# Performance work log

Measured on AMD Instinct MI355X. Metric: run time of the kernel, lower is better.

The kernel has to match this reference:

```python
import jax, jax.numpy as jnp
import numpy as np

NUM_USER = 50000
NUM_ITEM = 30000
N_NODES = NUM_USER + NUM_ITEM
N_EDGES = 1_000_000
FEAT_DIM = 768
DIM_LATENT = 128
DIM_ID = 64
NEG_SLOPE = 0.01  # F.leaky_relu default


def leaky_relu(x):
    return jnp.where(x >= 0, x, NEG_SLOPE * x)


def l2_normalize(x, eps=1e-12):
    # F.normalize(dim=-1): divide by clamped L2 norm
    n = jnp.sqrt(jnp.sum(x * x, axis=-1, keepdims=True))
    return x / jnp.maximum(n, eps)


def graph_gat(x, W, edge_index, num_nodes):
    """MGAT GraphGAT: x -> x@W, gated inner-product attention, softmax over
    incoming edges per destination node, scatter-add, L2 normalize."""
    x = x @ W                                    # [N, D]
    src = edge_index[0]                          # j (source)
    dst = edge_index[1]                          # i (target)
    x_j = x[src]                                 # [E, D]
    x_i = x[dst]                                 # [E, D]
    inner = jnp.sum(x_i * x_j, axis=-1)          # [E]
    # gate: sigmoid(deg(src)^-0.5 * inner)
    deg = jax.ops.segment_sum(jnp.ones_like(inner), src, num_segments=num_nodes)
    gate = jax.nn.sigmoid(deg[src] ** -0.5 * inner)
    score = inner * gate                         # [E]
    # segment softmax over destination nodes
    smax = jax.ops.segment_max(score, dst, num_segments=num_nodes)
    e = jnp.exp(score - smax[dst])
    denom = jax.ops.segment_sum(e, dst, num_segments=num_nodes)
    alpha = e / (denom[dst] + 1e-16)             # [E]
    out = jax.ops.segment_sum(x_j * alpha[:, None], dst, num_segments=num_nodes)
    return l2_normalize(out)


def setup_inputs() -> dict:
    key = jax.random.key(0)
    ks = jax.random.split(key, 16)

    def xavier(k, shape):
        fan_in, fan_out = shape[0], shape[1]
        std = float(np.sqrt(2.0 / (fan_in + fan_out)))
        return jax.random.normal(k, shape, dtype=jnp.float32) * std

    features = jax.random.normal(ks[0], (NUM_ITEM, FEAT_DIM), dtype=jnp.float32)
    id_embedding = jax.random.normal(ks[1], (N_NODES, DIM_ID), dtype=jnp.float32)
    # edge_index [2, E] with no self-loops (remove_self_loops is then identity)
    src = jax.random.randint(ks[2], (N_EDGES,), 0, N_NODES)
    off = jax.random.randint(ks[3], (N_EDGES,), 1, N_NODES)
    dst = (src + off) % N_NODES
    edge_index = jnp.stack([src, dst]).astype(jnp.int64)

    return {
        "features": features,
        "id_embedding": id_embedding,
        "edge_index": edge_index,
        "preference": xavier(ks[4], (NUM_USER, DIM_LATENT)),
        "mlp_w": xavier(ks[5], (FEAT_DIM, DIM_LATENT)),
        "mlp_b": jnp.zeros((DIM_LATENT,), dtype=jnp.float32),
        "conv1_w": xavier(ks[6], (DIM_LATENT, DIM_LATENT)),
        "lin1_w": xavier(ks[7], (DIM_LATENT, DIM_ID)),
        "lin1_b": jnp.zeros((DIM_ID,), dtype=jnp.float32),
        "g1_w": xavier(ks[8], (DIM_LATENT, DIM_ID)),
        "g1_b": jnp.zeros((DIM_ID,), dtype=jnp.float32),
        "conv2_w": xavier(ks[9], (DIM_ID, DIM_ID)),
        "lin2_w": xavier(ks[10], (DIM_ID, DIM_ID)),
        "lin2_b": jnp.zeros((DIM_ID,), dtype=jnp.float32),
        "g2_w": xavier(ks[11], (DIM_ID, DIM_ID)),
        "g2_b": jnp.zeros((DIM_ID,), dtype=jnp.float32),
    }


def reference(features, id_embedding, edge_index, preference, mlp_w, mlp_b,
              conv1_w, lin1_w, lin1_b, g1_w, g1_b,
              conv2_w, lin2_w, lin2_b, g2_w, g2_b):
    temp_features = jnp.tanh(features @ mlp_w + mlp_b)        # [num_item, dim_latent]
    x = jnp.concatenate([preference, temp_features], axis=0)  # [N, dim_latent]
    x = l2_normalize(x)

    h = leaky_relu(graph_gat(x, conv1_w, edge_index, N_NODES))
    x_hat = leaky_relu(x @ lin1_w + lin1_b) + id_embedding
    x1 = leaky_relu(h @ g1_w + g1_b + x_hat)                  # [N, dim_id]

    h = leaky_relu(graph_gat(x1, conv2_w, edge_index, N_NODES))
    x_hat = leaky_relu(x1 @ lin2_w + lin2_b) + id_embedding
    x2 = leaky_relu(h @ g2_w + g2_b + x_hat)                  # [N, dim_id]

    return jnp.concatenate([x1, x2], axis=1)                  # [N, 2*dim_id]
```

## Files before the change

### kernel.cpp

```cpp
#include <hip/hip_runtime.h>
#include <hip/hip_bf16.h>
#include <math.h>

#define NUM_USER 50000
#define NUM_ITEM 30000
#define N_NODES  80000
#define N_EDGES  1000000
#define FEAT_DIM 768
#define DLAT 128
#define DID  64
#define NEG_SLOPE 0.01f

#define SCAN_NB ((N_NODES + 255) / 256)

__device__ __forceinline__ float leaky(float v) { return v >= 0.f ? v : NEG_SLOPE * v; }

__device__ __forceinline__ float wave_reduce_sum(float v) {
#pragma unroll
    for (int off = 32; off > 0; off >>= 1) v += __shfl_xor(v, off, 64);
    return v;
}

__device__ __forceinline__ unsigned short f2bf(float f) {
    unsigned int u = __float_as_uint(f);
    unsigned int r = u + 0x7fffu + ((u >> 16) & 1u);
    return (unsigned short)(r >> 16);
}
__device__ __forceinline__ float bf2f(unsigned short h) {
    return __uint_as_float(((unsigned int)h) << 16);
}

template<int K_TOTAL, int N_COLS, int ACT, bool HAS_BIAS>
__global__ __launch_bounds__(256) void gemm_kernel(
    const float* __restrict__ A, int lda,
    const float* __restrict__ W, const float* __restrict__ bias,
    float* __restrict__ O, int ldo, int rows)
{
    constexpr int KC = 64;
    constexpr int CT = N_COLS / 16;
    __shared__ float sW[KC * N_COLS];
    __shared__ float sX[64][KC + 4];

    const int tid = threadIdx.x;
    const int ty = tid >> 4;
    const int tx = tid & 15;
    const int r0 = blockIdx.x * 64;

    float acc[4][CT];
#pragma unroll
    for (int i = 0; i < 4; i++)
#pragma unroll
        for (int c = 0; c < CT; c++) acc[i][c] = 0.f;

    for (int kc = 0; kc < K_TOTAL; kc += KC) {
        const float4* Wc = (const float4*)(W + (size_t)kc * N_COLS);
        for (int i = tid; i < KC * N_COLS / 4; i += 256)
            ((float4*)sW)[i] = Wc[i];
        {
            int row = tid >> 2, q = tid & 3;
            int gr = r0 + row;
            float4 v[4];
            if (gr < rows) {
                const float4* Ar = (const float4*)(A + (size_t)gr * lda + kc);
#pragma unroll
                for (int i = 0; i < 4; i++) v[i] = Ar[q * 4 + i];
            } else {
#pragma unroll
                for (int i = 0; i < 4; i++) v[i] = make_float4(0.f, 0.f, 0.f, 0.f);
            }
#pragma unroll
            for (int i = 0; i < 4; i++)
                *(float4*)&sX[row][q * 16 + i * 4] = v[i];
        }
        __syncthreads();

        for (int k = 0; k < KC; k++) {
            float xv[4];
#pragma unroll
            for (int i = 0; i < 4; i++) xv[i] = sX[ty * 4 + i][k];
            float4 w0 = *(const float4*)&sW[k * N_COLS + tx * CT];
            if (CT == 8) {
                float4 w1 = *(const float4*)&sW[k * N_COLS + tx * CT + 4];
#pragma unroll
                for (int i = 0; i < 4; i++) {
                    acc[i][0] += xv[i] * w0.x; acc[i][1] += xv[i] * w0.y;
                    acc[i][2] += xv[i] * w0.z; acc[i][3] += xv[i] * w0.w;
                    acc[i][4] += xv[i] * w1.x; acc[i][5] += xv[i] * w1.y;
                    acc[i][6] += xv[i] * w1.z; acc[i][7] += xv[i] * w1.w;
                }
            } else {
#pragma unroll
                for (int i = 0; i < 4; i++) {
                    acc[i][0] += xv[i] * w0.x; acc[i][1] += xv[i] * w0.y;
                    acc[i][2] += xv[i] * w0.z; acc[i][3] += xv[i] * w0.w;
                }
            }
        }
        __syncthreads();
    }

#pragma unroll
    for (int i = 0; i < 4; i++) {
        int gr = r0 + ty * 4 + i;
        if (gr >= rows) continue;
#pragma unroll
        for (int c = 0; c < CT; c++) {
            int col = tx * CT + c;
            float v = acc[i][c];
            if (HAS_BIAS) v += bias[col];
            if (ACT == 1) v = tanhf(v);
            O[(size_t)gr * ldo + col] = v;
        }
    }
}

typedef __attribute__((ext_vector_type(8))) short short8v;
typedef __attribute__((ext_vector_type(4))) float f32x4;

__global__ __launch_bounds__(256) void wt_prep_kernel(
    const float* __restrict__ W, unsigned short* __restrict__ Wh,
    unsigned short* __restrict__ Wl)
{
    int id = blockIdx.x * 256 + threadIdx.x;
    if (id < FEAT_DIM * DLAT) {
        int n = id / FEAT_DIM, k = id % FEAT_DIM;
        float v = W[(size_t)k * DLAT + n];
        unsigned short h = f2bf(v);
        Wh[id] = h;
        Wl[id] = f2bf(v - bf2f(h));
    }
}

__global__ __launch_bounds__(256) void mlp_mfma_kernel(
    const float* __restrict__ F,
    const unsigned short* __restrict__ Wh, const unsigned short* __restrict__ Wl,
    const float* __restrict__ bias, float* __restrict__ xout)
{
    __shared__ unsigned short sAh[64][72];
    __shared__ unsigned short sAl[64][72];
    __shared__ unsigned short sWh[128][72];
    __shared__ unsigned short sWlo[128][72];

    const int tid = threadIdx.x;
    const int lane = tid & 63;
    const int w = tid >> 6;
    const int wr = w >> 1, wc = w & 1;
    const int r0 = blockIdx.x * 64;

    f32x4 acc[2][4];
#pragma unroll
    for (int m = 0; m < 2; m++)
#pragma unroll
        for (int n = 0; n < 4; n++) acc[m][n] = (f32x4){0.f, 0.f, 0.f, 0.f};

    for (int kc = 0; kc < FEAT_DIM; kc += 64) {
#pragma unroll
        for (int it = 0; it < 2; it++) {
            int slot = tid + it * 256;
            int row = slot >> 3;
            int k8 = (slot & 7) * 8;
            int gr = r0 + row;
            float v[8];
#pragma unroll
            for (int i = 0; i < 8; i++) v[i] = 0.f;
            if (gr < NUM_ITEM) {
                const float4* p = (const float4*)(F + (size_t)gr * FEAT_DIM + kc + k8);
                float4 a = p[0], b = p[1];
                v[0]=a.x; v[1]=a.y; v[2]=a.z; v[3]=a.w;
                v[4]=b.x; v[5]=b.y; v[6]=b.z; v[7]=b.w;
            }
            unsigned int ph[4], pl[4];
#pragma unroll
            for (int i = 0; i < 4; i++) {
                unsigned short h0 = f2bf(v[2*i]),   l0 = f2bf(v[2*i]   - bf2f(h0));
                unsigned short h1 = f2bf(v[2*i+1]), l1 = f2bf(v[2*i+1] - bf2f(h1));
                ph[i] = (unsigned int)h0 | ((unsigned int)h1 << 16);
                pl[i] = (unsigned int)l0 | ((unsigned int)l1 << 16);
            }
            *(int4*)&sAh[row][k8] = make_int4((int)ph[0], (int)ph[1], (int)ph[2], (int)ph[3]);
            *(int4*)&sAl[row][k8] = make_int4((int)pl[0], (int)pl[1], (int)pl[2], (int)pl[3]);
        }
#pragma unroll
        for (int it = 0; it < 4; it++) {
            int slot = tid + it * 256;
            int n = slot >> 3;
            int k8 = (slot & 7) * 8;
            *(int4*)&sWh[n][k8]  = *(const int4*)(Wh + (size_t)n * FEAT_DIM + kc + k8);
            *(int4*)&sWlo[n][k8] = *(const int4*)(Wl + (size_t)n * FEAT_DIM + kc + k8);
        }
        __syncthreads();

#pragma unroll
        for (int k0 = 0; k0 < 64; k0 += 32) {
            int klane = k0 + (lane >> 4) * 8;
            short8v ah[2], al[2], bh[4], bl[4];
#pragma unroll
            for (int m = 0; m < 2; m++) {
                int row = wr * 32 + m * 16 + (lane & 15);
                ah[m] = *(const short8v*)&sAh[row][klane];
                al[m] = *(const short8v*)&sAl[row][klane];
            }
#pragma unroll
            for (int n = 0; n < 4; n++) {
                int col = wc * 64 + n * 16 + (lane & 15);
                bh[n] = *(const short8v*)&sWh[col][klane];
                bl[n] = *(const short8v*)&sWlo[col][klane];
            }
#pragma unroll
            for (int m = 0; m < 2; m++)
#pragma unroll
                for (int n = 0; n < 4; n++) {
                    acc[m][n] = __builtin_amdgcn_mfma_f32_16x16x32_bf16(ah[m], bh[n], acc[m][n], 0, 0, 0);
                    acc[m][n] = __builtin_amdgcn_mfma_f32_16x16x32_bf16(ah[m], bl[n], acc[m][n], 0, 0, 0);
                    acc[m][n] = __builtin_amdgcn_mfma_f32_16x16x32_bf16(al[m], bh[n], acc[m][n], 0, 0, 0);
                }
        }
        __syncthreads();
    }

#pragma unroll
    for (int m = 0; m < 2; m++) {
        int rbase = r0 + wr * 32 + m * 16 + (lane >> 4) * 4;
#pragma unroll
        for (int n = 0; n < 4; n++) {
            int col = wc * 64 + n * 16 + (lane & 15);
            float bv = bias[col];
#pragma unroll
            for (int q = 0; q < 4; q++) {
                int gr = rbase + q;
                if (gr < NUM_ITEM)
                    xout[(size_t)gr * DLAT + col] = tanhf(acc[m][n][q] + bv);
            }
        }
    }
}

template<int K>
__global__ __launch_bounds__(256) void combine_gemm_kernel(
    const float* __restrict__ H,
    const float* __restrict__ X, int ldx,
    const float* __restrict__ g_w, const float* __restrict__ g_b,
    const float* __restrict__ lin_w, const float* __restrict__ lin_b,
    const float* __restrict__ id_emb,
    float* __restrict__ out, int out_off)
{
    constexpr int KC = 64;
    __shared__ float sWg[KC * DID];
    __shared__ float sWl[KC * DID];
    __shared__ float sH[64][KC + 4];
    __shared__ float sX[64][KC + 4];

    const int tid = threadIdx.x;
    const int ty = tid >> 4;
    const int tx = tid & 15;
    const int r0 = blockIdx.x * 64;

    float accG[4][4], accL[4][4];
#pragma unroll
    for (int i = 0; i < 4; i++)
#pragma unroll
        for (int c = 0; c < 4; c++) { accG[i][c] = 0.f; accL[i][c] = 0.f; }

    for (int kc = 0; kc < K; kc += KC) {
        const float4* Wg = (const float4*)(g_w + (size_t)kc * DID);
        const float4* Wl = (const float4*)(lin_w + (size_t)kc * DID);
        for (int i = tid; i < KC * DID / 4; i += 256) {
            ((float4*)sWg)[i] = Wg[i];
            ((float4*)sWl)[i] = Wl[i];
        }
        {
            int row = tid >> 2, q = tid & 3;
            int gr = r0 + row;
            const float4* Hr = (const float4*)(H + (size_t)gr * K + kc);
            const float4* Xr = (const float4*)(X + (size_t)gr * ldx + kc);
#pragma unroll
            for (int i = 0; i < 4; i++) {
                *(float4*)&sH[row][q * 16 + i * 4] = Hr[q * 4 + i];
                *(float4*)&sX[row][q * 16 + i * 4] = Xr[q * 4 + i];
            }
        }
        __syncthreads();

        for (int k = 0; k < KC; k++) {
            float hv[4], xv[4];
#pragma unroll
            for (int i = 0; i < 4; i++) { hv[i] = sH[ty * 4 + i][k]; xv[i] = sX[ty * 4 + i][k]; }
            float4 wg = *(const float4*)&sWg[k * DID + tx * 4];
            float4 wl = *(const float4*)&sWl[k * DID + tx * 4];
#pragma unroll
            for (int i = 0; i < 4; i++) {
                accG[i][0] += hv[i] * wg.x; accG[i][1] += hv[i] * wg.y;
                accG[i][2] += hv[i] * wg.z; accG[i][3] += hv[i] * wg.w;
                accL[i][0] += xv[i] * wl.x; accL[i][1] += xv[i] * wl.y;
                accL[i][2] += xv[i] * wl.z; accL[i][3] += xv[i] * wl.w;
            }
        }
        __syncthreads();
    }

#pragma unroll
    for (int i = 0; i < 4; i++) {
        int gr = r0 + ty * 4 + i;
#pragma unroll
        for (int c = 0; c < 4; c++) {
            int col = tx * 4 + c;
            float xh = leaky(accL[i][c] + lin_b[col]) + id_emb[(size_t)gr * DID + col];
            float v = leaky(accG[i][c] + g_b[col] + xh);
            out[(size_t)gr * (2 * DID) + out_off + col] = v;
        }
    }
}

__global__ __launch_bounds__(256) void l2norm_rows_kernel(float* __restrict__ x)
{
    int wid = blockIdx.x * 4 + (threadIdx.x >> 6);
    if (wid >= N_NODES) return;
    int lane = threadIdx.x & 63;
    float* row = x + (size_t)wid * DLAT;
    float v0 = row[lane], v1 = row[lane + 64];
    float s = wave_reduce_sum(v0 * v0 + v1 * v1);
    float inv = 1.0f / fmaxf(sqrtf(s), 1e-12f);
    row[lane] = v0 * inv;
    row[lane + 64] = v1 * inv;
}

__global__ __launch_bounds__(256) void count_kernel(
    const int* __restrict__ src, const int* __restrict__ dst,
    int* __restrict__ deg_out, int* __restrict__ cnt_in)
{
    int e = blockIdx.x * 256 + threadIdx.x;
    if (e < N_EDGES) {
        atomicAdd(&deg_out[src[e]], 1);
        atomicAdd(&cnt_in[dst[e]], 1);
    }
}

__global__ __launch_bounds__(256) void scan_local_kernel(
    const int* __restrict__ cnt, int* __restrict__ rowptr, int* __restrict__ blocksum)
{
    __shared__ int wsum[4];
    int gid = blockIdx.x * 256 + threadIdx.x;
    int lane = threadIdx.x & 63, w = threadIdx.x >> 6;
    int orig = (gid < N_NODES) ? cnt[gid] : 0;
    int v = orig;
#pragma unroll
    for (int off = 1; off < 64; off <<= 1) {
        int u = __shfl_up(v, off, 64);
        if (lane >= off) v += u;
    }
    if (lane == 63) wsum[w] = v;
    __syncthreads();
    int woff = 0;
#pragma unroll
    for (int i = 0; i < 4; i++) woff += (i < w) ? wsum[i] : 0;
    if (gid < N_NODES) rowptr[gid] = v - orig + woff;
    if (threadIdx.x == 255) blocksum[blockIdx.x] = woff + v;
}

__global__ __launch_bounds__(512) void scan_blocksums_kernel(int* __restrict__ blocksum)
{
    __shared__ int s[512];
    int t = threadIdx.x;
    int orig = (t < SCAN_NB) ? blocksum[t] : 0;
    s[t] = orig;
    __syncthreads();
    for (int off = 1; off < 512; off <<= 1) {
        int u = (t >= off) ? s[t - off] : 0;
        __syncthreads();
        s[t] += u;
        __syncthreads();
    }
    if (t < SCAN_NB) blocksum[t] = s[t] - orig;
}

__global__ __launch_bounds__(256) void scan_add_kernel(
    int* __restrict__ rowptr, const int* __restrict__ blocksum)
{
    int gid = blockIdx.x * 256 + threadIdx.x;
    if (gid < N_NODES) rowptr[gid] += blocksum[blockIdx.x];
    if (gid == 0) rowptr[N_NODES] = N_EDGES;
}

__global__ __launch_bounds__(256) void csr_fill_kernel(
    const int* __restrict__ src, const int* __restrict__ dst,
    const int* __restrict__ rowptr, int* __restrict__ cursor, int* __restrict__ csr_src)
{
    int e = blockIdx.x * 256 + threadIdx.x;
    if (e < N_EDGES) {
        int d = dst[e];
        int slot = rowptr[d] + atomicAdd(&cursor[d], 1);
        csr_src[slot] = src[e];
    }
}

__global__ __launch_bounds__(256) void deg_rsqrt_kernel(
    const int* __restrict__ deg_out, float* __restrict__ rsq)
{
    int n = blockIdx.x * 256 + threadIdx.x;
    if (n < N_NODES) rsq[n] = rsqrtf((float)deg_out[n]);
}

template<int D>
__global__ __launch_bounds__(256) void gat_layer_kernel(
    const float* __restrict__ xw, const int* __restrict__ rowptr,
    const int* __restrict__ csr_src, const float* __restrict__ rsq_deg,
    float* __restrict__ h)
{
    constexpr int SG  = D / 8;
    constexpr int EPC = 64 / SG;
    int wid = blockIdx.x * 4 + (threadIdx.x >> 6);
    if (wid >= N_NODES) return;
    const int lane = threadIdx.x & 63;
    const int g = lane / SG;
    const int t = lane % SG;
    const int start = rowptr[wid], end = rowptr[wid + 1];

    const float* xdp = xw + (size_t)wid * D + 8 * t;
    float4 xd0 = *(const float4*)(xdp);
    float4 xd1 = *(const float4*)(xdp + 4);

    float m = -1e30f, l = 0.f;
    float acc[8];
#pragma unroll
    for (int c = 0; c < 8; c++) acc[c] = 0.f;

    for (int base = start; base < end; base += EPC) {
        int i = base + g;
        bool valid = (i < end);
        int s = valid ? csr_src[i] : 0;
        const float* row = xw + (size_t)s * D + 8 * t;
        float4 a0 = *(const float4*)(row);
        float4 a1 = *(const float4*)(row + 4);
        float p = a0.x * xd0.x + a0.y * xd0.y + a0.z * xd0.z + a0.w * xd0.w
                + a1.x * xd1.x + a1.y * xd1.y + a1.z * xd1.z + a1.w * xd1.w;
#pragma unroll
        for (int off = SG / 2; off > 0; off >>= 1) p += __shfl_xor(p, off, 64);
        float rsd = valid ? rsq_deg[s] : 1.f;
        float gate = 1.0f / (1.0f + __expf(-(p * rsd)));
        float sc = valid ? p * gate : -1e30f;
        float mnew = fmaxf(m, sc);
        float scale = __expf(m - mnew);
        float w = valid ? __expf(sc - mnew) : 0.f;
        l = l * scale + w;
        acc[0] = acc[0] * scale + w * a0.x;
        acc[1] = acc[1] * scale + w * a0.y;
        acc[2] = acc[2] * scale + w * a0.z;
        acc[3] = acc[3] * scale + w * a0.w;
        acc[4] = acc[4] * scale + w * a1.x;
        acc[5] = acc[5] * scale + w * a1.y;
        acc[6] = acc[6] * scale + w * a1.z;
        acc[7] = acc[7] * scale + w * a1.w;
        m = mnew;
    }

#pragma unroll
    for (int off = SG; off < 64; off <<= 1) {
        float mo = __shfl_xor(m, off, 64);
        float lo = __shfl_xor(l, off, 64);
        float mnew = fmaxf(m, mo);
        float s1 = __expf(m - mnew), s2 = __expf(mo - mnew);
        l = l * s1 + lo * s2;
#pragma unroll
        for (int c = 0; c < 8; c++) {
            float ao = __shfl_xor(acc[c], off, 64);
            acc[c] = acc[c] * s1 + ao * s2;
        }
        m = mnew;
    }

    float invl = 1.0f / (l + 1e-16f);
    float ss = 0.f;
#pragma unroll
    for (int c = 0; c < 8; c++) { acc[c] *= invl; ss += acc[c] * acc[c]; }
#pragma unroll
    for (int off = SG / 2; off > 0; off >>= 1) ss += __shfl_xor(ss, off, 64);
    float inv = 1.0f / fmaxf(sqrtf(ss), 1e-12f);

    if (g == 0) {
        float4 o0, o1;
        o0.x = leaky(acc[0] * inv); o0.y = leaky(acc[1] * inv);
        o0.z = leaky(acc[2] * inv); o0.w = leaky(acc[3] * inv);
        o1.x = leaky(acc[4] * inv); o1.y = leaky(acc[5] * inv);
        o1.z = leaky(acc[6] * inv); o1.w = leaky(acc[7] * inv);
        float* op = h + (size_t)wid * D + 8 * t;
        *(float4*)(op) = o0;
        *(float4*)(op + 4) = o1;
    }
}

extern "C" void kernel_launch(void* const* d_in, const int* in_sizes, int n_in,
                              void* d_out, int out_size, void* d_ws, size_t ws_size,
                              hipStream_t stream)
{
    const float* features = (const float*)d_in[0];
    const float* id_emb   = (const float*)d_in[1];
    const int*   ei       = (const int*)d_in[2];
    const float* pref     = (const float*)d_in[3];
    const float* mlp_w    = (const float*)d_in[4];
    const float* mlp_b    = (const float*)d_in[5];
    const float* conv1_w  = (const float*)d_in[6];
    const float* lin1_w   = (const float*)d_in[7];
    const float* lin1_b   = (const float*)d_in[8];
    const float* g1_w     = (const float*)d_in[9];
    const float* g1_b     = (const float*)d_in[10];
    const float* conv2_w  = (const float*)d_in[11];
    const float* lin2_w   = (const float*)d_in[12];
    const float* lin2_b   = (const float*)d_in[13];
    const float* g2_w     = (const float*)d_in[14];
    const float* g2_b     = (const float*)d_in[15];
    const int* src = ei;
    const int* dst = ei + N_EDGES;
    float* out = (float*)d_out;

    float* x       = (float*)d_ws;
    float* xw      = x   + (size_t)N_NODES * DLAT;
    float* gat     = xw  + (size_t)N_NODES * DLAT;
    int*   deg_out = (int*)(gat + (size_t)N_NODES * DLAT);
    int*   cnt     = deg_out + N_NODES;
    int*   rowptr  = cnt + N_NODES;
    int*   csr_src = rowptr + N_NODES + 1;
    int*   blocksum = csr_src + N_EDGES;
    float* rsq_deg = (float*)cnt;
    unsigned short* Wh = (unsigned short*)gat;
    unsigned short* Wl = Wh + (size_t)FEAT_DIM * DLAT;

    hipMemsetAsync(deg_out, 0, N_NODES * sizeof(int), stream);
    hipMemsetAsync(cnt, 0, N_NODES * sizeof(int), stream);
    count_kernel<<<(N_EDGES + 255) / 256, 256, 0, stream>>>(src, dst, deg_out, cnt);
    scan_local_kernel<<<SCAN_NB, 256, 0, stream>>>(cnt, rowptr, blocksum);
    scan_blocksums_kernel<<<1, 512, 0, stream>>>(blocksum);
    scan_add_kernel<<<SCAN_NB, 256, 0, stream>>>(rowptr, blocksum);
    hipMemsetAsync(cnt, 0, N_NODES * sizeof(int), stream);
    csr_fill_kernel<<<(N_EDGES + 255) / 256, 256, 0, stream>>>(src, dst, rowptr, cnt, csr_src);
    deg_rsqrt_kernel<<<(N_NODES + 255) / 256, 256, 0, stream>>>(deg_out, rsq_deg);

    hipMemcpyAsync(x, pref, (size_t)NUM_USER * DLAT * sizeof(float),
                   hipMemcpyDeviceToDevice, stream);
    wt_prep_kernel<<<(FEAT_DIM * DLAT + 255) / 256, 256, 0, stream>>>(mlp_w, Wh, Wl);
    mlp_mfma_kernel<<<(NUM_ITEM + 63) / 64, 256, 0, stream>>>(
        features, Wh, Wl, mlp_b, x + (size_t)NUM_USER * DLAT);
    l2norm_rows_kernel<<<(N_NODES + 3) / 4, 256, 0, stream>>>(x);

    gemm_kernel<DLAT, DLAT, 0, false><<<N_NODES / 64, 256, 0, stream>>>(
        x, DLAT, conv1_w, nullptr, xw, DLAT, N_NODES);
    gat_layer_kernel<DLAT><<<(N_NODES + 3) / 4, 256, 0, stream>>>(
        xw, rowptr, csr_src, rsq_deg, gat);
    combine_gemm_kernel<DLAT><<<N_NODES / 64, 256, 0, stream>>>(
        gat, x, DLAT, g1_w, g1_b, lin1_w, lin1_b, id_emb, out, 0);

    gemm_kernel<DID, DID, 0, false><<<N_NODES / 64, 256, 0, stream>>>(
        out, 2 * DID, conv2_w, nullptr, xw, DID, N_NODES);
    gat_layer_kernel<DID><<<(N_NODES + 3) / 4, 256, 0, stream>>>(
        xw, rowptr, csr_src, rsq_deg, gat);
    combine_gemm_kernel<DID><<<N_NODES / 64, 256, 0, stream>>>(
        gat, out, 2 * DID, g2_w, g2_b, lin2_w, lin2_b, id_emb, out, DID);
}
```

Before: 515.1 us.

## Move conv and combine GEMMs to split-bf16 MFMA kernels

Replaces the scalar FP32 shared-memory GEMMs for the conv1/conv2 projections and the fused lin/gate combine step with MFMA kernels. These use a three-term hi/lo bf16 split to keep near-FP32 accuracy. All small weight matrices are pre-transposed and split into bf16 hi/lo buffers placed in extra workspace after the CSR arrays. B fragments are read straight from global memory rather than staged in LDS. The aim is to cut FP32 FMA cost, at the price of three times the MFMA work plus extra prep launches.

Measured after the change: 517.8 us. No clear change (+0.5%).

```diff
diff --git a/kernel.cpp b/kernel.cpp
--- a/kernel.cpp
+++ b/kernel.cpp
@@ -30,104 +30,192 @@
     return __uint_as_float(((unsigned int)h) << 16);
 }
 
-template<int K_TOTAL, int N_COLS, int ACT, bool HAS_BIAS>
-__global__ __launch_bounds__(256) void gemm_kernel(
-    const float* __restrict__ A, int lda,
-    const float* __restrict__ W, const float* __restrict__ bias,
-    float* __restrict__ O, int ldo, int rows)
-{
-    constexpr int KC = 64;
-    constexpr int CT = N_COLS / 16;
-    __shared__ float sW[KC * N_COLS];
-    __shared__ float sX[64][KC + 4];
-
-    const int tid = threadIdx.x;
-    const int ty = tid >> 4;
-    const int tx = tid & 15;
-    const int r0 = blockIdx.x * 64;
-
-    float acc[4][CT];
-#pragma unroll
-    for (int i = 0; i < 4; i++)
-#pragma unroll
-        for (int c = 0; c < CT; c++) acc[i][c] = 0.f;
-
-    for (int kc = 0; kc < K_TOTAL; kc += KC) {
-        const float4* Wc = (const float4*)(W + (size_t)kc * N_COLS);
-        for (int i = tid; i < KC * N_COLS / 4; i += 256)
-            ((float4*)sW)[i] = Wc[i];
-        {
-            int row = tid >> 2, q = tid & 3;
-            int gr = r0 + row;
-            float4 v[4];
-            if (gr < rows) {
-                const float4* Ar = (const float4*)(A + (size_t)gr * lda + kc);
-#pragma unroll
-                for (int i = 0; i < 4; i++) v[i] = Ar[q * 4 + i];
-            } else {
-#pragma unroll
-                for (int i = 0; i < 4; i++) v[i] = make_float4(0.f, 0.f, 0.f, 0.f);
-            }
-#pragma unroll
-            for (int i = 0; i < 4; i++)
-                *(float4*)&sX[row][q * 16 + i * 4] = v[i];
-        }
-        __syncthreads();
-
-        for (int k = 0; k < KC; k++) {
-            float xv[4];
-#pragma unroll
-            for (int i = 0; i < 4; i++) xv[i] = sX[ty * 4 + i][k];
-            float4 w0 = *(const float4*)&sW[k * N_COLS + tx * CT];
-            if (CT == 8) {
-                float4 w1 = *(const float4*)&sW[k * N_COLS + tx * CT + 4];
-#pragma unroll
-                for (int i = 0; i < 4; i++) {
-                    acc[i][0] += xv[i] * w0.x; acc[i][1] += xv[i] * w0.y;
-                    acc[i][2] += xv[i] * w0.z; acc[i][3] += xv[i] * w0.w;
-                    acc[i][4] += xv[i] * w1.x; acc[i][5] += xv[i] * w1.y;
-                    acc[i][6] += xv[i] * w1.z; acc[i][7] += xv[i] * w1.w;
-                }
-            } else {
-#pragma unroll
-                for (int i = 0; i < 4; i++) {
-                    acc[i][0] += xv[i] * w0.x; acc[i][1] += xv[i] * w0.y;
-                    acc[i][2] += xv[i] * w0.z; acc[i][3] += xv[i] * w0.w;
-                }
-            }
-        }
-        __syncthreads();
-    }
-
-#pragma unroll
-    for (int i = 0; i < 4; i++) {
-        int gr = r0 + ty * 4 + i;
-        if (gr >= rows) continue;
-#pragma unroll
-        for (int c = 0; c < CT; c++) {
-            int col = tx * CT + c;
-            float v = acc[i][c];
-            if (HAS_BIAS) v += bias[col];
-            if (ACT == 1) v = tanhf(v);
-            O[(size_t)gr * ldo + col] = v;
-        }
-    }
-}
-
 typedef __attribute__((ext_vector_type(8))) short short8v;
 typedef __attribute__((ext_vector_type(4))) float f32x4;
 
-__global__ __launch_bounds__(256) void wt_prep_kernel(
+__device__ __forceinline__ void split_store8(
+    float4 a, float4 b, unsigned short* dh, unsigned short* dl)
+{
+    float v[8] = {a.x, a.y, a.z, a.w, b.x, b.y, b.z, b.w};
+    unsigned int ph[4], pl[4];
+#pragma unroll
+    for (int i = 0; i < 4; i++) {
+        unsigned short h0 = f2bf(v[2*i]),   l0 = f2bf(v[2*i]   - bf2f(h0));
+        unsigned short h1 = f2bf(v[2*i+1]), l1 = f2bf(v[2*i+1] - bf2f(h1));
+        ph[i] = (unsigned int)h0 | ((unsigned int)h1 << 16);
+        pl[i] = (unsigned int)l0 | ((unsigned int)l1 << 16);
+    }
+    *(int4*)dh = make_int4((int)ph[0], (int)ph[1], (int)ph[2], (int)ph[3]);
+    *(int4*)dl = make_int4((int)pl[0], (int)pl[1], (int)pl[2], (int)pl[3]);
+}
+
+template<int KK, int NN>
+__global__ __launch_bounds__(256) void wt_prep_g_kernel(
     const float* __restrict__ W, unsigned short* __restrict__ Wh,
     unsigned short* __restrict__ Wl)
 {
     int id = blockIdx.x * 256 + threadIdx.x;
-    if (id < FEAT_DIM * DLAT) {
-        int n = id / FEAT_DIM, k = id % FEAT_DIM;
-        float v = W[(size_t)k * DLAT + n];
+    if (id < KK * NN) {
+        int n = id / KK, k = id % KK;
+        float v = W[(size_t)k * NN + n];
         unsigned short h = f2bf(v);
         Wh[id] = h;
         Wl[id] = f2bf(v - bf2f(h));
+    }
+}
+
+template<int K, int NC>
+__global__ __launch_bounds__(256) void conv_mfma_kernel(
+    const float* __restrict__ X, int ldx,
+    const unsigned short* __restrict__ Wth, const unsigned short* __restrict__ Wtl,
+    float* __restrict__ O, int ldo)
+{
+    constexpr int NW = NC / 64;
+    constexpr int MW = 4 / NW;
+    constexpr int WROWS = 64 / MW;
+    constexpr int MF = WROWS / 16;
+    constexpr int KSTEPS = K / 32;
+    constexpr int KP = K + 8;
+
+    __shared__ unsigned short sAh[64][KP];
+    __shared__ unsigned short sAl[64][KP];
+
+    const int tid = threadIdx.x;
+    const int lane = tid & 63;
+    const int w = tid >> 6;
+    const int wr = w / NW, wc = w % NW;
+    const int r0 = blockIdx.x * 64;
+
+#pragma unroll
+    for (int it = 0; it < K / 32; it++) {
+        int slot = tid + it * 256;
+        int row = slot / (K / 8);
+        int k8 = (slot % (K / 8)) * 8;
+        const float4* p = (const float4*)(X + (size_t)(r0 + row) * ldx + k8);
+        split_store8(p[0], p[1], &sAh[row][k8], &sAl[row][k8]);
+    }
+    __syncthreads();
+
+    f32x4 acc[MF][4];
+#pragma unroll
+    for (int m = 0; m < MF; m++)
+#pragma unroll
+        for (int n = 0; n < 4; n++) acc[m][n] = (f32x4){0.f, 0.f, 0.f, 0.f};
+
+#pragma unroll
+    for (int ks = 0; ks < KSTEPS; ks++) {
+        int klane = ks * 32 + (lane >> 4) * 8;
+        short8v ah[MF], al[MF];
+#pragma unroll
+        for (int m = 0; m < MF; m++) {
+            int row = wr * WROWS + m * 16 + (lane & 15);
+            ah[m] = *(const short8v*)&sAh[row][klane];
+            al[m] = *(const short8v*)&sAl[row][klane];
+        }
+#pragma unroll
+        for (int n = 0; n < 4; n++) {
+            int col = wc * 64 + n * 16 + (lane & 15);
+            short8v bh = *(const short8v*)(Wth + (size_t)col * K + klane);
+            short8v bl = *(const short8v*)(Wtl + (size_t)col * K + klane);
+#pragma unroll
+            for (int m = 0; m < MF; m++) {
+                acc[m][n] = __builtin_amdgcn_mfma_f32_16x16x32_bf16(ah[m], bh, acc[m][n], 0, 0, 0);
+                acc[m][n] = __builtin_amdgcn_mfma_f32_16x16x32_bf16(ah[m], bl, acc[m][n], 0, 0, 0);
+                acc[m][n] = __builtin_amdgcn_mfma_f32_16x16x32_bf16(al[m], bh, acc[m][n], 0, 0, 0);
+            }
+        }
+    }
+
+#pragma unroll
+    for (int m = 0; m < MF; m++) {
+        int rbase = r0 + wr * WROWS + m * 16 + (lane >> 4) * 4;
+#pragma unroll
+        for (int n = 0; n < 4; n++) {
+            int col = wc * 64 + n * 16 + (lane & 15);
+#pragma unroll
+            for (int q = 0; q < 4; q++)
+                O[(size_t)(rbase + q) * ldo + col] = acc[m][n][q];
+        }
+    }
+}
+
+template<int K>
+__global__ __launch_bounds__(256) void combine_mfma_kernel(
+    const float* __restrict__ H, int ldh,
+    const float* __restrict__ X, int ldx,
+    const unsigned short* __restrict__ Gth, const unsigned short* __restrict__ Gtl,
+    const unsigned short* __restrict__ Lth, const unsigned short* __restrict__ Ltl,
+    const float* __restrict__ g_b, const float* __restrict__ lin_b,
+    const float* __restrict__ id_emb, float* __restrict__ out, int out_off)
+{
+    constexpr int KSTEPS = K / 32;
+    constexpr int KP = K + 8;
+
+    __shared__ unsigned short sHh[64][KP];
+    __shared__ unsigned short sHl[64][KP];
+    __shared__ unsigned short sXh[64][KP];
+    __shared__ unsigned short sXl[64][KP];
+
+    const int tid = threadIdx.x;
+    const int lane = tid & 63;
+    const int wr = tid >> 6;
+    const int r0 = blockIdx.x * 64;
+
+#pragma unroll
+    for (int it = 0; it < K / 32; it++) {
+        int slot = tid + it * 256;
+        int row = slot / (K / 8);
+        int k8 = (slot % (K / 8)) * 8;
+        const float4* ph = (const float4*)(H + (size_t)(r0 + row) * ldh + k8);
+        split_store8(ph[0], ph[1], &sHh[row][k8], &sHl[row][k8]);
+        const float4* px = (const float4*)(X + (size_t)(r0 + row) * ldx + k8);
+        split_store8(px[0], px[1], &sXh[row][k8], &sXl[row][k8]);
+    }
+    __syncthreads();
+
+    f32x4 accG[4], accL[4];
+#pragma unroll
+    for (int n = 0; n < 4; n++) {
+        accG[n] = (f32x4){0.f, 0.f, 0.f, 0.f};
+        accL[n] = (f32x4){0.f, 0.f, 0.f, 0.f};
+    }
+
+#pragma unroll
+    for (int ks = 0; ks < KSTEPS; ks++) {
+        int klane = ks * 32 + (lane >> 4) * 8;
+        int row = wr * 16 + (lane & 15);
+        short8v hh = *(const short8v*)&sHh[row][klane];
+        short8v hl = *(const short8v*)&sHl[row][klane];
+        short8v xh = *(const short8v*)&sXh[row][klane];
+        short8v xl = *(const short8v*)&sXl[row][klane];
+#pragma unroll
+        for (int n = 0; n < 4; n++) {
+            int col = n * 16 + (lane & 15);
+            short8v gh = *(const short8v*)(Gth + (size_t)col * K + klane);
+            short8v gl = *(const short8v*)(Gtl + (size_t)col * K + klane);
+            short8v lh = *(const short8v*)(Lth + (size_t)col * K + klane);
+            short8v ll = *(const short8v*)(Ltl + (size_t)col * K + klane);
+            accG[n] = __builtin_amdgcn_mfma_f32_16x16x32_bf16(hh, gh, accG[n], 0, 0, 0);
+            accG[n] = __builtin_amdgcn_mfma_f32_16x16x32_bf16(hh, gl, accG[n], 0, 0, 0);
+            accG[n] = __builtin_amdgcn_mfma_f32_16x16x32_bf16(hl, gh, accG[n], 0, 0, 0);
+            accL[n] = __builtin_amdgcn_mfma_f32_16x16x32_bf16(xh, lh, accL[n], 0, 0, 0);
+            accL[n] = __builtin_amdgcn_mfma_f32_16x16x32_bf16(xh, ll, accL[n], 0, 0, 0);
+            accL[n] = __builtin_amdgcn_mfma_f32_16x16x32_bf16(xl, lh, accL[n], 0, 0, 0);
+        }
+    }
+
+    int rbase = r0 + wr * 16 + (lane >> 4) * 4;
+#pragma unroll
+    for (int n = 0; n < 4; n++) {
+        int col = n * 16 + (lane & 15);
+        float gb = g_b[col], lb = lin_b[col];
+#pragma unroll
+        for (int q = 0; q < 4; q++) {
+            int gr = rbase + q;
+            float xhv = leaky(accL[n][q] + lb) + id_emb[(size_t)gr * DID + col];
+            float v = leaky(accG[n][q] + gb + xhv);
+            out[(size_t)gr * (2 * DID) + out_off + col] = v;
+        }
     }
 }
 
@@ -160,25 +248,12 @@
             int row = slot >> 3;
             int k8 = (slot & 7) * 8;
             int gr = r0 + row;
-            float v[8];
-#pragma unroll
-            for (int i = 0; i < 8; i++) v[i] = 0.f;
+            float4 a = make_float4(0.f, 0.f, 0.f, 0.f), b = a;
             if (gr < NUM_ITEM) {
                 const float4* p = (const float4*)(F + (size_t)gr * FEAT_DIM + kc + k8);
-                float4 a = p[0], b = p[1];
-                v[0]=a.x; v[1]=a.y; v[2]=a.z; v[3]=a.w;
-                v[4]=b.x; v[5]=b.y; v[6]=b.z; v[7]=b.w;
+                a = p[0]; b = p[1];
             }
-            unsigned int ph[4], pl[4];
-#pragma unroll
-            for (int i = 0; i < 4; i++) {
-                unsigned short h0 = f2bf(v[2*i]),   l0 = f2bf(v[2*i]   - bf2f(h0));
-                unsigned short h1 = f2bf(v[2*i+1]), l1 = f2bf(v[2*i+1] - bf2f(h1));
-                ph[i] = (unsigned int)h0 | ((unsigned int)h1 << 16);
-                pl[i] = (unsigned int)l0 | ((unsigned int)l1 << 16);
-            }
-            *(int4*)&sAh[row][k8] = make_int4((int)ph[0], (int)ph[1], (int)ph[2], (int)ph[3]);
-            *(int4*)&sAl[row][k8] = make_int4((int)pl[0], (int)pl[1], (int)pl[2], (int)pl[3]);
+            split_store8(a, b, &sAh[row][k8], &sAl[row][k8]);
         }
 #pragma unroll
         for (int it = 0; it < 4; it++) {
@@ -231,82 +306,6 @@
                 if (gr < NUM_ITEM)
                     xout[(size_t)gr * DLAT + col] = tanhf(acc[m][n][q] + bv);
             }
-        }
-    }
-}
-
-template<int K>
-__global__ __launch_bounds__(256) void combine_gemm_kernel(
-    const float* __restrict__ H,
-    const float* __restrict__ X, int ldx,
-    const float* __restrict__ g_w, const float* __restrict__ g_b,
-    const float* __restrict__ lin_w, const float* __restrict__ lin_b,
-    const float* __restrict__ id_emb,
-    float* __restrict__ out, int out_off)
-{
-    constexpr int KC = 64;
-    __shared__ float sWg[KC * DID];
-    __shared__ float sWl[KC * DID];
-    __shared__ float sH[64][KC + 4];
-    __shared__ float sX[64][KC + 4];
-
-    const int tid = threadIdx.x;
-    const int ty = tid >> 4;
-    const int tx = tid & 15;
-    const int r0 = blockIdx.x * 64;
-
-    float accG[4][4], accL[4][4];
-#pragma unroll
-    for (int i = 0; i < 4; i++)
-#pragma unroll
-        for (int c = 0; c < 4; c++) { accG[i][c] = 0.f; accL[i][c] = 0.f; }
-
-    for (int kc = 0; kc < K; kc += KC) {
-        const float4* Wg = (const float4*)(g_w + (size_t)kc * DID);
-        const float4* Wl = (const float4*)(lin_w + (size_t)kc * DID);
-        for (int i = tid; i < KC * DID / 4; i += 256) {
-            ((float4*)sWg)[i] = Wg[i];
-            ((float4*)sWl)[i] = Wl[i];
-        }
-        {
-            int row = tid >> 2, q = tid & 3;
-            int gr = r0 + row;
-            const float4* Hr = (const float4*)(H + (size_t)gr * K + kc);
-            const float4* Xr = (const float4*)(X + (size_t)gr * ldx + kc);
-#pragma unroll
-            for (int i = 0; i < 4; i++) {
-                *(float4*)&sH[row][q * 16 + i * 4] = Hr[q * 4 + i];
-                *(float4*)&sX[row][q * 16 + i * 4] = Xr[q * 4 + i];
-            }
-        }
-        __syncthreads();
-
-        for (int k = 0; k < KC; k++) {
-            float hv[4], xv[4];
-#pragma unroll
-            for (int i = 0; i < 4; i++) { hv[i] = sH[ty * 4 + i][k]; xv[i] = sX[ty * 4 + i][k]; }
-            float4 wg = *(const float4*)&sWg[k * DID + tx * 4];
-            float4 wl = *(const float4*)&sWl[k * DID + tx * 4];
-#pragma unroll
-            for (int i = 0; i < 4; i++) {
-                accG[i][0] += hv[i] * wg.x; accG[i][1] += hv[i] * wg.y;
-                accG[i][2] += hv[i] * wg.z; accG[i][3] += hv[i] * wg.w;
-                accL[i][0] += xv[i] * wl.x; accL[i][1] += xv[i] * wl.y;
-                accL[i][2] += xv[i] * wl.z; accL[i][3] += xv[i] * wl.w;
-            }
-        }
-        __syncthreads();
-    }
-
-#pragma unroll
-    for (int i = 0; i < 4; i++) {
-        int gr = r0 + ty * 4 + i;
-#pragma unroll
-        for (int c = 0; c < 4; c++) {
-            int col = tx * 4 + c;
-            float xh = leaky(accL[i][c] + lin_b[col]) + id_emb[(size_t)gr * DID + col];
-            float v = leaky(accG[i][c] + g_b[col] + xh);
-            out[(size_t)gr * (2 * DID) + out_off + col] = v;
         }
     }
 }
@@ -521,8 +520,30 @@
     int*   csr_src = rowptr + N_NODES + 1;
     int*   blocksum = csr_src + N_EDGES;
     float* rsq_deg = (float*)cnt;
-    unsigned short* Wh = (unsigned short*)gat;
-    unsigned short* Wl = Wh + (size_t)FEAT_DIM * DLAT;
+    unsigned short* mlpWh = (unsigned short*)gat;
+    unsigned short* mlpWl = mlpWh + (size_t)FEAT_DIM * DLAT;
+    unsigned short* wbase = (unsigned short*)(
+        (((uintptr_t)(blocksum + SCAN_NB)) + 15) & ~(uintptr_t)15);
+    unsigned short* wc1h = wbase;
+    unsigned short* wc1l = wc1h + 16384;
+    unsigned short* wl1h = wc1l + 16384;
+    unsigned short* wl1l = wl1h + 8192;
+    unsigned short* wg1h = wl1l + 8192;
+    unsigned short* wg1l = wg1h + 8192;
+    unsigned short* wc2h = wg1l + 8192;
+    unsigned short* wc2l = wc2h + 4096;
+    unsigned short* wl2h = wc2l + 4096;
+    unsigned short* wl2l = wl2h + 4096;
+    unsigned short* wg2h = wl2l + 4096;
+    unsigned short* wg2l = wg2h + 4096;
+
+    wt_prep_g_kernel<FEAT_DIM, DLAT><<<384, 256, 0, stream>>>(mlp_w, mlpWh, mlpWl);
+    wt_prep_g_kernel<DLAT, DLAT><<<64, 256, 0, stream>>>(conv1_w, wc1h, wc1l);
+    wt_prep_g_kernel<DLAT, DID><<<32, 256, 0, stream>>>(lin1_w, wl1h, wl1l);
+    wt_prep_g_kernel<DLAT, DID><<<32, 256, 0, stream>>>(g1_w, wg1h, wg1l);
+    wt_prep_g_kernel<DID, DID><<<16, 256, 0, stream>>>(conv2_w, wc2h, wc2l);
+    wt_prep_g_kernel<DID, DID><<<16, 256, 0, stream>>>(lin2_w, wl2h, wl2l);
+    wt_prep_g_kernel<DID, DID><<<16, 256, 0, stream>>>(g2_w, wg2h, wg2l);
 
     hipMemsetAsync(deg_out, 0, N_NODES * sizeof(int), stream);
     hipMemsetAsync(cnt, 0, N_NODES * sizeof(int), stream);
@@ -536,22 +557,21 @@
 
     hipMemcpyAsync(x, pref, (size_t)NUM_USER * DLAT * sizeof(float),
                    hipMemcpyDeviceToDevice, stream);
-    wt_prep_kernel<<<(FEAT_DIM * DLAT + 255) / 256, 256, 0, stream>>>(mlp_w, Wh, Wl);
     mlp_mfma_kernel<<<(NUM_ITEM + 63) / 64, 256, 0, stream>>>(
-        features, Wh, Wl, mlp_b, x + (size_t)NUM_USER * DLAT);
+        features, mlpWh, mlpWl, mlp_b, x + (size_t)NUM_USER * DLAT);
     l2norm_rows_kernel<<<(N_NODES + 3) / 4, 256, 0, stream>>>(x);
 
-    gemm_kernel<DLAT, DLAT, 0, false><<<N_NODES / 64, 256, 0, stream>>>(
-        x, DLAT, conv1_w, nullptr, xw, DLAT, N_NODES);
+    conv_mfma_kernel<DLAT, DLAT><<<N_NODES / 64, 256, 0, stream>>>(
+        x, DLAT, wc1h, wc1l, xw, DLAT);
     gat_layer_kernel<DLAT><<<(N_NODES + 3) / 4, 256, 0, stream>>>(
         xw, rowptr, csr_src, rsq_deg, gat);
-    combine_gemm_kernel<DLAT><<<N_NODES / 64, 256, 0, stream>>>(
-        gat, x, DLAT, g1_w, g1_b, lin1_w, lin1_b, id_emb, out, 0);
-
-    gemm_kernel<DID, DID, 0, false><<<N_NODES / 64, 256, 0, stream>>>(
-        out, 2 * DID, conv2_w, nullptr, xw, DID, N_NODES);
+    combine_mfma_kernel<DLAT><<<N_NODES / 64, 256, 0, stream>>>(
+        gat, DLAT, x, DLAT, wg1h, wg1l, wl1h, wl1l, g1_b, lin1_b, id_emb, out, 0);
+
+    conv_mfma_kernel<DID, DID><<<N_NODES / 64, 256, 0, stream>>>(
+        out, 2 * DID, wc2h, wc2l, xw, DID);
     gat_layer_kernel<DID><<<(N_NODES + 3) / 4, 256, 0, stream>>>(
         xw, rowptr, csr_src, rsq_deg, gat);
-    combine_gemm_kernel<DID><<<N_NODES / 64, 256, 0, stream>>>(
-        gat, out, 2 * DID, g2_w, g2_b, lin2_w, lin2_b, id_emb, out, DID);
-}
+    combine_mfma_kernel<DID><<<N_NODES / 64, 256, 0, stream>>>(
+        gat, DID, out, 2 * DID, wg2h, wg2l, wl2h, wl2l, g2_b, lin2_b, id_emb, out, DID);
+}
```
